# Kernel tuning notes

Hardware: AMD Instinct MI355X
Metric: run time of the kernel (lower is better)

Reference implementation:

```python
import jax, jax.numpy as jnp
import numpy as np

N_NODES = 100000
N_EDGES = 3200000
D_IN = 256
D_OUT = 256


def setup_inputs() -> dict:
    key = jax.random.key(0)
    k1, k2, k3, k4, k5 = jax.random.split(key, 5)
    inputs = jax.random.normal(k1, (N_NODES, D_IN), dtype=jnp.float32)
    # Glorot-uniform init as in _glorot_init
    init_range = np.sqrt(6.0 / (D_IN + D_OUT)).astype(np.float32)
    weight = jax.random.uniform(k2, (D_IN, D_OUT), dtype=jnp.float32,
                                minval=-init_range, maxval=init_range)
    edge_src = jax.random.randint(k3, (N_EDGES,), 0, N_NODES, dtype=jnp.int32)
    edge_dst = jax.random.randint(k4, (N_EDGES,), 0, N_NODES, dtype=jnp.int32)
    # normalized adjacency values (positive, like D^-1/2 A D^-1/2 entries)
    edge_vals = jax.random.uniform(k5, (N_EDGES,), dtype=jnp.float32)
    return {"inputs": inputs, "weight": weight, "edge_src": edge_src,
            "edge_dst": edge_dst, "edge_vals": edge_vals}


def reference(inputs, weight, edge_src, edge_dst, edge_vals):
    # x = inputs @ W          : [N, D_OUT]
    x = inputs @ weight
    # SpMM: out[d] = sum_{e: dst(e)=d} vals[e] * x[src(e)]
    msgs = edge_vals[:, None] * x[edge_src]          # [E, D_OUT]
    out = jax.ops.segment_sum(msgs, edge_dst, num_segments=inputs.shape[0])
    return jax.nn.relu(out)
```

## Files before the change

### kernel.cpp

```cpp
#include <hip/hip_runtime.h>

#define N_NODES 100000
#define N_EDGES 3200000
#define DDIM 256
#define NB 1563
#define BIN_BLK 256
#define CHUNK (N_EDGES / BIN_BLK)
#define TB 1024

typedef short s16x8 __attribute__((ext_vector_type(8)));
typedef float f32x4 __attribute__((ext_vector_type(4)));
typedef float f32x2 __attribute__((ext_vector_type(2)));

__device__ __forceinline__ unsigned short f32_to_bf16(float f) {
    union { float f; unsigned int u; } c; c.f = f;
    unsigned int u = c.u;
    unsigned int r = u + 0x7fffu + ((u >> 16) & 1u);
    return (unsigned short)(r >> 16);
}
__device__ __forceinline__ float bl16(unsigned int u) {
    union { unsigned int x; float f; } c; c.x = u << 16; return c.f;
}
__device__ __forceinline__ float bh16(unsigned int u) {
    union { unsigned int x; float f; } c; c.x = u & 0xffff0000u; return c.f;
}

__global__ __launch_bounds__(256) void prep_w(const float* __restrict__ W,
                                              unsigned short* __restrict__ Wt) {
    __shared__ float tile[32][33];
    const int tx = threadIdx.x & 31;
    const int ty = threadIdx.x >> 5;
    const int n0 = blockIdx.x * 32;
    const int k0 = blockIdx.y * 32;
    for (int i = 0; i < 32; i += 8)
        tile[ty + i][tx] = W[(size_t)(k0 + ty + i) * DDIM + n0 + tx];
    __syncthreads();
    for (int i = 0; i < 32; i += 8)
        Wt[(size_t)(n0 + ty + i) * DDIM + k0 + tx] = f32_to_bf16(tile[tx][ty + i]);
}

__global__ __launch_bounds__(256) void gemm_mfma(const float* __restrict__ A,
                                                 const unsigned short* __restrict__ Wt,
                                                 unsigned short* __restrict__ Xb) {
    __shared__ unsigned short As[64][DDIM + 8];
    const int tid = threadIdx.x;
    const int rowBase = blockIdx.x * 64;

#pragma unroll
    for (int p = 0; p < 16; ++p) {
        const int flat = p * 256 + tid;
        const int row = flat >> 6;
        const int k4 = (flat & 63) * 4;
        const int gr = rowBase + row;
        float4 v = make_float4(0.f, 0.f, 0.f, 0.f);
        if (gr < N_NODES) v = *(const float4*)&A[(size_t)gr * DDIM + k4];
        ushort4 h;
        h.x = f32_to_bf16(v.x); h.y = f32_to_bf16(v.y);
        h.z = f32_to_bf16(v.z); h.w = f32_to_bf16(v.w);
        *(ushort4*)&As[row][k4] = h;
    }
    __syncthreads();

    const int wave = tid >> 6;
    const int lane = tid & 63;
    const int lrow = lane & 15;
    const int quad = lane >> 4;
    const int cb = wave * 64;

    f32x4 acc[4][4] = {};

#pragma unroll
    for (int ks = 0; ks < 8; ++ks) {
        const int k0 = ks * 32 + quad * 8;
        s16x8 a[4], b[4];
#pragma unroll
        for (int ri = 0; ri < 4; ++ri)
            a[ri] = *(const s16x8*)&As[ri * 16 + lrow][k0];
#pragma unroll
        for (int ci = 0; ci < 4; ++ci)
            b[ci] = *(const s16x8*)&Wt[(size_t)(cb + ci * 16 + lrow) * DDIM + k0];
#pragma unroll
        for (int ri = 0; ri < 4; ++ri)
#pragma unroll
            for (int ci = 0; ci < 4; ++ci)
                acc[ri][ci] = __builtin_amdgcn_mfma_f32_16x16x32_bf16(a[ri], b[ci], acc[ri][ci], 0, 0, 0);
    }

    __syncthreads();
#pragma unroll
    for (int ri = 0; ri < 4; ++ri)
#pragma unroll
        for (int rr = 0; rr < 4; ++rr)
#pragma unroll
            for (int ci = 0; ci < 4; ++ci)
                As[ri * 16 + quad * 4 + rr][cb + ci * 16 + lrow] =
                    f32_to_bf16(acc[ri][ci][rr]);
    __syncthreads();

#pragma unroll
    for (int it = 0; it < 8; ++it) {
        const int flat = it * 256 + tid;
        const int row  = flat >> 5;
        const int c8   = (flat & 31) * 8;
        const int grow = rowBase + row;
        if (grow < N_NODES)
            *(s16x8*)&Xb[(size_t)grow * DDIM + c8] = *(const s16x8*)&As[row][c8];
    }
}

__global__ __launch_bounds__(TB) void hist_coarse(const int* __restrict__ edst,
                                                  int* __restrict__ gcounts) {
    __shared__ int h[NB];
    const int tid = threadIdx.x;
    for (int i = tid; i < NB; i += TB) h[i] = 0;
    __syncthreads();
    const int lo = blockIdx.x * CHUNK;
    const int hi = lo + CHUNK;
    for (int e = lo + tid; e < hi; e += TB) atomicAdd(&h[edst[e] >> 6], 1);
    __syncthreads();
    for (int i = tid; i < NB; i += TB)
        if (h[i]) atomicAdd(&gcounts[i], h[i]);
}

__global__ __launch_bounds__(256) void scan_coarse(const int* __restrict__ gcounts,
                                                   int* __restrict__ bbase,
                                                   int* __restrict__ bcursor,
                                                   int* __restrict__ off) {
    __shared__ int part[256];
    const int t = threadIdx.x;
    const int chunk = (NB + 255) / 256;
    const int lo = t * chunk;
    const int hi = min(lo + chunk, NB);
    int s = 0;
    for (int i = lo; i < hi; ++i) s += gcounts[i];
    part[t] = s;
    __syncthreads();
    for (int d = 1; d < 256; d <<= 1) {
        int a = (t >= d) ? part[t - d] : 0;
        __syncthreads();
        part[t] += a;
        __syncthreads();
    }
    int run = part[t] - s;
    for (int i = lo; i < hi; ++i) {
        bbase[i] = run;
        bcursor[i] = run;
        run += gcounts[i];
    }
    if (t == 255) {
        bbase[NB] = run;
        off[N_NODES] = run;
    }
}

__global__ __launch_bounds__(TB) void bin_coarse(const int* __restrict__ esrc,
                                                 const int* __restrict__ edst,
                                                 const float* __restrict__ evals,
                                                 int* __restrict__ bcursor,
                                                 long long* __restrict__ tmp) {
    __shared__ int h[NB];
    __shared__ int sb[NB];
    const int tid = threadIdx.x;
    for (int i = tid; i < NB; i += TB) h[i] = 0;
    __syncthreads();
    const int lo = blockIdx.x * CHUNK;
    const int hi = lo + CHUNK;
    for (int e = lo + tid; e < hi; e += TB) atomicAdd(&h[edst[e] >> 6], 1);
    __syncthreads();
    for (int i = tid; i < NB; i += TB)
        sb[i] = h[i] ? atomicAdd(&bcursor[i], h[i]) : 0;
    __syncthreads();
    for (int e = lo + tid; e < hi; e += TB) {
        const int d = edst[e];
        const int b = d >> 6;
        const int p = atomicAdd(&sb[b], 1);
        const unsigned int lo32 = (unsigned int)(esrc[e] | ((d & 63) << 17));
        const unsigned int hi32 = (unsigned int)__float_as_int(evals[e]);
        tmp[p] = (long long)(((unsigned long long)hi32 << 32) | lo32);
    }
}

__global__ __launch_bounds__(TB) void refine(const long long* __restrict__ tmp,
                                             const int* __restrict__ bbase,
                                             int* __restrict__ off,
                                             long long* __restrict__ srcval) {
    __shared__ int nh[64];
    __shared__ int nb[64];
    const int b = blockIdx.x;
    const int tid = threadIdx.x;
    const int base = bbase[b];
    const int cnt = bbase[b + 1] - base;
    const int n0 = b * 64;
    const int nn = min(64, N_NODES - n0);
    if (tid < 64) nh[tid] = 0;
    __syncthreads();
    for (int i = tid; i < cnt; i += TB) {
        const long long q = tmp[base + i];
        atomicAdd(&nh[((int)(unsigned int)q) >> 17], 1);
    }
    __syncthreads();
    if (tid == 0) {
        int run = 0;
        for (int i = 0; i < 64; ++i) { nb[i] = run; run += nh[i]; }
    }
    __syncthreads();
    if (tid < nn) off[n0 + tid] = base + nb[tid];
    __syncthreads();
    for (int i = tid; i < cnt; i += TB) {
        const long long q = tmp[base + i];
        const unsigned int lo32 = (unsigned int)q;
        const int dl = (int)(lo32 >> 17);
        const int p = atomicAdd(&nb[dl], 1);
        srcval[base + p] = (long long)((q & 0xFFFFFFFF00000000ull) | (lo32 & 0x1FFFF));
    }
}

#define HEDGE(q) { a0 += v##q * bl16(h##q); a1 += v##q * bh16(h##q); }

__global__ __launch_bounds__(256) void spmm_half(const unsigned short* __restrict__ xb,
                                                 const int* __restrict__ off,
                                                 const long long* __restrict__ srcval,
                                                 float* __restrict__ out) {
    const int node = blockIdx.x * 4 + (threadIdx.x >> 6);
    const int lane = threadIdx.x & 63;
    const int dimoff = blockIdx.y << 7;
    const int start = off[node];
    const int end = off[node + 1];

    const unsigned short* xcol = xb + dimoff + lane * 2;
    float a0 = 0.f, a1 = 0.f;

    for (int base = start; base < end; base += 64) {
        const int cnt = min(64, end - base);
        int s_l = 0;
        float v_l = 0.f;
        if (lane < cnt) {
            const long long q = __builtin_nontemporal_load(&srcval[base + lane]);
            s_l = (int)((unsigned int)q & 0x1FFFF);
            v_l = __int_as_float((int)(q >> 32));
        }
        int j = 0;
        for (; j + 8 <= cnt; j += 8) {
            const int s0 = __shfl(s_l, j + 0);
            const int s1 = __shfl(s_l, j + 1);
            const int s2 = __shfl(s_l, j + 2);
            const int s3 = __shfl(s_l, j + 3);
            const int s4 = __shfl(s_l, j + 4);
            const int s5 = __shfl(s_l, j + 5);
            const int s6 = __shfl(s_l, j + 6);
            const int s7 = __shfl(s_l, j + 7);
            const float v0 = __shfl(v_l, j + 0);
            const float v1 = __shfl(v_l, j + 1);
            const float v2 = __shfl(v_l, j + 2);
            const float v3 = __shfl(v_l, j + 3);
            const float v4 = __shfl(v_l, j + 4);
            const float v5 = __shfl(v_l, j + 5);
            const float v6 = __shfl(v_l, j + 6);
            const float v7 = __shfl(v_l, j + 7);
            const unsigned int h0 = *(const unsigned int*)&xcol[(size_t)s0 * DDIM];
            const unsigned int h1 = *(const unsigned int*)&xcol[(size_t)s1 * DDIM];
            const unsigned int h2 = *(const unsigned int*)&xcol[(size_t)s2 * DDIM];
            const unsigned int h3 = *(const unsigned int*)&xcol[(size_t)s3 * DDIM];
            const unsigned int h4 = *(const unsigned int*)&xcol[(size_t)s4 * DDIM];
            const unsigned int h5 = *(const unsigned int*)&xcol[(size_t)s5 * DDIM];
            const unsigned int h6 = *(const unsigned int*)&xcol[(size_t)s6 * DDIM];
            const unsigned int h7 = *(const unsigned int*)&xcol[(size_t)s7 * DDIM];
            HEDGE(0) HEDGE(1) HEDGE(2) HEDGE(3)
            HEDGE(4) HEDGE(5) HEDGE(6) HEDGE(7)
        }
        for (; j < cnt; ++j) {
            const int s = __shfl(s_l, j);
            const float v = __shfl(v_l, j);
            const unsigned int h = *(const unsigned int*)&xcol[(size_t)s * DDIM];
            a0 += v * bl16(h); a1 += v * bh16(h);
        }
    }

    f32x2 o;
    o[0] = fmaxf(a0, 0.f);
    o[1] = fmaxf(a1, 0.f);
    __builtin_nontemporal_store(o, (f32x2*)&out[(size_t)node * DDIM + dimoff + lane * 2]);
}
#undef HEDGE

extern "C" void kernel_launch(void* const* d_in, const int* in_sizes, int n_in,
                              void* d_out, int out_size, void* d_ws, size_t ws_size,
                              hipStream_t stream) {
    const float* inputs = (const float*)d_in[0];
    const float* weight = (const float*)d_in[1];
    const int* esrc     = (const int*)d_in[2];
    const int* edst     = (const int*)d_in[3];
    const float* evals  = (const float*)d_in[4];
    float* out = (float*)d_out;

    unsigned short* xb = (unsigned short*)d_ws;
    unsigned short* Wt = xb + (size_t)N_NODES * DDIM;
    int* off     = (int*)(Wt + DDIM * DDIM);
    int* gcounts = off + N_NODES + 1;
    int* bbase   = gcounts + NB;
    int* bcursor = bbase + NB + 1;
    uintptr_t a  = ((uintptr_t)(bcursor + NB) + 15) & ~(uintptr_t)15;
    long long* tmp    = (long long*)a;
    long long* srcval = tmp + N_EDGES;

    prep_w<<<dim3(8, 8), 256, 0, stream>>>(weight, Wt);

    gemm_mfma<<<(N_NODES + 63) / 64, 256, 0, stream>>>(inputs, Wt, xb);

    (void)hipMemsetAsync(gcounts, 0, NB * sizeof(int), stream);
    hist_coarse<<<BIN_BLK, TB, 0, stream>>>(edst, gcounts);
    scan_coarse<<<1, 256, 0, stream>>>(gcounts, bbase, bcursor, off);
    bin_coarse<<<BIN_BLK, TB, 0, stream>>>(esrc, edst, evals, bcursor, tmp);
    refine<<<NB, TB, 0, stream>>>(tmp, bbase, off, srcval);

    spmm_half<<<dim3(N_NODES / 4, 2), 256, 0, stream>>>(xb, off, srcval, out);
}
```

Measured before the change: 548.3 us.

## Fuse CSR build stages into one cooperative kernel with grid syncs

```diff
diff --git a/kernel.cpp b/kernel.cpp
--- a/kernel.cpp
+++ b/kernel.cpp
@@ -1,4 +1,7 @@
 #include <hip/hip_runtime.h>
+#include <hip/hip_cooperative_groups.h>
+
+namespace cg = cooperative_groups;
 
 #define N_NODES 100000
 #define N_EDGES 3200000
@@ -108,65 +111,63 @@
     }
 }
 
-__global__ __launch_bounds__(TB) void hist_coarse(const int* __restrict__ edst,
-                                                  int* __restrict__ gcounts) {
+__global__ __launch_bounds__(TB) void build_csr(const int* __restrict__ esrc,
+                                                const int* __restrict__ edst,
+                                                const float* __restrict__ evals,
+                                                int* __restrict__ gcounts,
+                                                int* __restrict__ bbase,
+                                                int* __restrict__ bcursor,
+                                                int* __restrict__ off,
+                                                long long* __restrict__ tmp,
+                                                long long* __restrict__ srcval) {
     __shared__ int h[NB];
+    __shared__ int sb[NB];
+    __shared__ int part[TB];
+    cg::grid_group grid = cg::this_grid();
     const int tid = threadIdx.x;
+    const int blk = blockIdx.x;
+    const int lo = blk * CHUNK;
+    const int hi = lo + CHUNK;
+
+    for (int i = blk * TB + tid; i < NB; i += gridDim.x * TB) gcounts[i] = 0;
+
     for (int i = tid; i < NB; i += TB) h[i] = 0;
-    __syncthreads();
-    const int lo = blockIdx.x * CHUNK;
-    const int hi = lo + CHUNK;
+    grid.sync();
     for (int e = lo + tid; e < hi; e += TB) atomicAdd(&h[edst[e] >> 6], 1);
     __syncthreads();
     for (int i = tid; i < NB; i += TB)
         if (h[i]) atomicAdd(&gcounts[i], h[i]);
-}
-
-__global__ __launch_bounds__(256) void scan_coarse(const int* __restrict__ gcounts,
-                                                   int* __restrict__ bbase,
-                                                   int* __restrict__ bcursor,
-                                                   int* __restrict__ off) {
-    __shared__ int part[256];
-    const int t = threadIdx.x;
-    const int chunk = (NB + 255) / 256;
-    const int lo = t * chunk;
-    const int hi = min(lo + chunk, NB);
-    int s = 0;
-    for (int i = lo; i < hi; ++i) s += gcounts[i];
-    part[t] = s;
-    __syncthreads();
-    for (int d = 1; d < 256; d <<= 1) {
-        int a = (t >= d) ? part[t - d] : 0;
-        __syncthreads();
-        part[t] += a;
-        __syncthreads();
-    }
-    int run = part[t] - s;
-    for (int i = lo; i < hi; ++i) {
-        bbase[i] = run;
-        bcursor[i] = run;
-        run += gcounts[i];
-    }
-    if (t == 255) {
-        bbase[NB] = run;
-        off[N_NODES] = run;
-    }
-}
-
-__global__ __launch_bounds__(TB) void bin_coarse(const int* __restrict__ esrc,
-                                                 const int* __restrict__ edst,
-                                                 const float* __restrict__ evals,
-                                                 int* __restrict__ bcursor,
-                                                 long long* __restrict__ tmp) {
-    __shared__ int h[NB];
-    __shared__ int sb[NB];
-    const int tid = threadIdx.x;
-    for (int i = tid; i < NB; i += TB) h[i] = 0;
-    __syncthreads();
-    const int lo = blockIdx.x * CHUNK;
-    const int hi = lo + CHUNK;
-    for (int e = lo + tid; e < hi; e += TB) atomicAdd(&h[edst[e] >> 6], 1);
-    __syncthreads();
+
+    grid.sync();
+
+    if (blk == 0) {
+        const int chunk = (NB + TB - 1) / TB;
+        const int lo2 = tid * chunk;
+        const int hi2 = min(lo2 + chunk, NB);
+        int s = 0;
+        for (int i = lo2; i < hi2; ++i) s += gcounts[i];
+        part[tid] = s;
+        __syncthreads();
+        for (int d = 1; d < TB; d <<= 1) {
+            int a = (tid >= d) ? part[tid - d] : 0;
+            __syncthreads();
+            part[tid] += a;
+            __syncthreads();
+        }
+        int run = part[tid] - s;
+        for (int i = lo2; i < hi2; ++i) {
+            bbase[i] = run;
+            bcursor[i] = run;
+            run += gcounts[i];
+        }
+        if (tid == TB - 1) {
+            bbase[NB] = run;
+            off[N_NODES] = run;
+        }
+    }
+
+    grid.sync();
+
     for (int i = tid; i < NB; i += TB)
         sb[i] = h[i] ? atomicAdd(&bcursor[i], h[i]) : 0;
     __syncthreads();
@@ -178,40 +179,38 @@
         const unsigned int hi32 = (unsigned int)__float_as_int(evals[e]);
         tmp[p] = (long long)(((unsigned long long)hi32 << 32) | lo32);
     }
-}
-
-__global__ __launch_bounds__(TB) void refine(const long long* __restrict__ tmp,
-                                             const int* __restrict__ bbase,
-                                             int* __restrict__ off,
-                                             long long* __restrict__ srcval) {
-    __shared__ int nh[64];
-    __shared__ int nb[64];
-    const int b = blockIdx.x;
-    const int tid = threadIdx.x;
-    const int base = bbase[b];
-    const int cnt = bbase[b + 1] - base;
-    const int n0 = b * 64;
-    const int nn = min(64, N_NODES - n0);
-    if (tid < 64) nh[tid] = 0;
-    __syncthreads();
-    for (int i = tid; i < cnt; i += TB) {
-        const long long q = tmp[base + i];
-        atomicAdd(&nh[((int)(unsigned int)q) >> 17], 1);
-    }
-    __syncthreads();
-    if (tid == 0) {
-        int run = 0;
-        for (int i = 0; i < 64; ++i) { nb[i] = run; run += nh[i]; }
-    }
-    __syncthreads();
-    if (tid < nn) off[n0 + tid] = base + nb[tid];
-    __syncthreads();
-    for (int i = tid; i < cnt; i += TB) {
-        const long long q = tmp[base + i];
-        const unsigned int lo32 = (unsigned int)q;
-        const int dl = (int)(lo32 >> 17);
-        const int p = atomicAdd(&nb[dl], 1);
-        srcval[base + p] = (long long)((q & 0xFFFFFFFF00000000ull) | (lo32 & 0x1FFFF));
+
+    grid.sync();
+
+    int* nh = h;
+    int* nbc = sb;
+    for (int b = blk; b < NB; b += gridDim.x) {
+        const int base = bbase[b];
+        const int cnt = bbase[b + 1] - base;
+        const int n0 = b * 64;
+        const int nn = min(64, N_NODES - n0);
+        __syncthreads();
+        if (tid < 64) nh[tid] = 0;
+        __syncthreads();
+        for (int i = tid; i < cnt; i += TB) {
+            const long long q = tmp[base + i];
+            atomicAdd(&nh[((int)(unsigned int)q) >> 17], 1);
+        }
+        __syncthreads();
+        if (tid == 0) {
+            int run = 0;
+            for (int i = 0; i < 64; ++i) { nbc[i] = run; run += nh[i]; }
+        }
+        __syncthreads();
+        if (tid < nn) off[n0 + tid] = base + nbc[tid];
+        __syncthreads();
+        for (int i = tid; i < cnt; i += TB) {
+            const long long q = tmp[base + i];
+            const unsigned int lo32 = (unsigned int)q;
+            const int dl = (int)(lo32 >> 17);
+            const int p = atomicAdd(&nbc[dl], 1);
+            srcval[base + p] = (long long)((q & 0xFFFFFFFF00000000ull) | (lo32 & 0x1FFFF));
+        }
     }
 }
 
@@ -307,11 +306,14 @@
 
     gemm_mfma<<<(N_NODES + 63) / 64, 256, 0, stream>>>(inputs, Wt, xb);
 
-    (void)hipMemsetAsync(gcounts, 0, NB * sizeof(int), stream);
-    hist_coarse<<<BIN_BLK, TB, 0, stream>>>(edst, gcounts);
-    scan_coarse<<<1, 256, 0, stream>>>(gcounts, bbase, bcursor, off);
-    bin_coarse<<<BIN_BLK, TB, 0, stream>>>(esrc, edst, evals, bcursor, tmp);
-    refine<<<NB, TB, 0, stream>>>(tmp, bbase, off, srcval);
+    {
+        void* args[] = { (void*)&esrc, (void*)&edst, (void*)&evals,
+                         (void*)&gcounts, (void*)&bbase, (void*)&bcursor,
+                         (void*)&off, (void*)&tmp, (void*)&srcval };
+        (void)hipLaunchCooperativeKernel((const void*)build_csr,
+                                         dim3(BIN_BLK), dim3(TB),
+                                         args, 0, stream);
+    }
 
     spmm_half<<<dim3(N_NODES / 4, 2), 256, 0, stream>>>(xb, off, srcval, out);
 }
```

New measurement: 662.8 us. +20.9%, slower.
